# Performance work log

Measured on AMD Instinct MI355X. Metric: run time of the kernel, lower is better.

The kernel has to match this reference:

```python
import jax, jax.numpy as jnp
import numpy as np

DIM = 64
HEAD_DIM = 4
NUM_HEADS = DIM // HEAD_DIM  # 16
ATTN_DIM = NUM_HEADS * HEAD_DIM  # 64
BN_EPS = 1e-5


def setup_inputs() -> dict:
    key = jax.random.key(0)
    k_x, k_qkv, k_proj, k_g, k_b, k_m, k_v = jax.random.split(key, 7)
    B, C, H, W = 8, DIM, 64, 64
    x = jax.random.normal(k_x, (B, C, H, W), dtype=jnp.float32)
    # nn.Linear(dim, 3*attn_dim, bias=False): y = x @ W^T; store transposed for x @ w
    w_qkv = jax.random.normal(k_qkv, (DIM, 3 * ATTN_DIM), dtype=jnp.float32) * (DIM ** -0.5)
    w_proj = jax.random.normal(k_proj, (ATTN_DIM, DIM), dtype=jnp.float32) * (ATTN_DIM ** -0.5)
    gamma = 1.0 + 0.1 * jax.random.normal(k_g, (DIM,), dtype=jnp.float32)
    beta = 0.1 * jax.random.normal(k_b, (DIM,), dtype=jnp.float32)
    bn_mean = 0.1 * jax.random.normal(k_m, (DIM,), dtype=jnp.float32)
    bn_var = jnp.abs(jax.random.normal(k_v, (DIM,), dtype=jnp.float32)) + 0.5
    return {"x": x, "w_qkv": w_qkv, "w_proj": w_proj, "gamma": gamma,
            "beta": beta, "bn_mean": bn_mean, "bn_var": bn_var}


def _forward(x, w_qkv, w_proj, gamma, beta, bn_mean, bn_var):
    B, C, H, W = x.shape
    Hp, Wp = H // 2, W // 2
    N = Hp * Wp
    # ---- MaxPool2d(2,2) with indices (non-overlapping windows) ----
    xr = x.reshape(B, C, Hp, 2, Wp, 2).transpose(0, 1, 2, 4, 3, 5).reshape(B, C, Hp, Wp, 4)
    idx = jnp.argmax(xr, axis=-1)              # [B,C,Hp,Wp] window-local argmax
    pooled = jnp.max(xr, axis=-1)              # [B,C,Hp,Wp]
    # ---- GA attention on pooled map ----
    t = pooled.transpose(0, 2, 3, 1).reshape(B, N, C)          # [B,N,C]
    qkv = (t @ w_qkv).reshape(B, N, 3, NUM_HEADS, HEAD_DIM)
    q, k, v = qkv[:, :, 0], qkv[:, :, 1], qkv[:, :, 2]          # [B,N,h,d]
    scale = HEAD_DIM ** -0.5
    attn = jnp.einsum('bnhd,bmhd->bhnm', q, k) * scale          # [B,h,N,N]
    attn = jax.nn.softmax(attn, axis=-1)
    o = jnp.einsum('bhnm,bmhd->bnhd', attn, v).reshape(B, N, ATTN_DIM)
    o = (o @ w_proj).reshape(B, Hp, Wp, C).transpose(0, 3, 1, 2)  # [B,C,Hp,Wp]
    # ---- BatchNorm2d (eval mode, running stats) ----
    inv = gamma / jnp.sqrt(bn_var + BN_EPS)
    o = o * inv[:, None, None] + (beta - bn_mean * inv)[:, None, None]
    # ---- MaxUnpool2d(2,2): scatter to argmax positions ----
    oh = jax.nn.one_hot(idx, 4, dtype=o.dtype)                  # [B,C,Hp,Wp,4]
    up = oh * o[..., None]
    out = up.reshape(B, C, Hp, Wp, 2, 2).transpose(0, 1, 2, 4, 3, 5).reshape(B, C, H, W)
    return out


def reference(x, w_qkv, w_proj, gamma, beta, bn_mean, bn_var):
    return _forward(x, w_qkv, w_proj, gamma, beta, bn_mean, bn_var)
```

## Files before the change

kernel.cpp:

```cpp
#include <hip/hip_runtime.h>
#include <hip/hip_bf16.h>


typedef float    f32x4 __attribute__((ext_vector_type(4)));
typedef _Float16 f16x8 __attribute__((ext_vector_type(8)));
typedef unsigned int uint32_tt;

static __device__ __forceinline__ uint32_tt pk2(float a, float b) {
    uint32_tt lo = (uint32_tt)__builtin_bit_cast(unsigned short, (_Float16)a);
    uint32_tt hi = (uint32_tt)__builtin_bit_cast(unsigned short, (_Float16)b);
    return lo | (hi << 16);
}

__global__ __launch_bounds__(256) void pool_kernel(const float* __restrict__ x,
                                                   float* __restrict__ t,
                                                   int* __restrict__ idx) {
    int g = blockIdx.x * 256 + threadIdx.x;
    int wp = g & 31, hp = (g >> 5) & 31, c = (g >> 10) & 63, b = g >> 16;
    const float* px = x + (((b * 64 + c) * 64 + 2 * hp) * 64 + 2 * wp);
    float2 r0 = *(const float2*)px;
    float2 r1 = *(const float2*)(px + 64);
    float best = r0.x; int bi = 0;
    if (r0.y > best) { best = r0.y; bi = 1; }
    if (r1.x > best) { best = r1.x; bi = 2; }
    if (r1.y > best) { best = r1.y; bi = 3; }
    int n = hp * 32 + wp;
    t[(b * 64 + c) * 1024 + n] = best;
    idx[g] = bi;
}

__global__ __launch_bounds__(192) void qkv_kernel(const float* __restrict__ t,
                                                  const float* __restrict__ w_qkv,
                                                  float* __restrict__ q,
                                                  float* __restrict__ k,
                                                  float* __restrict__ v) {
    __shared__ float trow[16 * 68];
    int tid = threadIdx.x;
    int row0 = blockIdx.x * 16;
    {
        int b0 = row0 >> 10, n0 = row0 & 1023;
        for (int i = tid; i < 1024; i += 192) {
            int c = i >> 4, nn = i & 15;
            trow[nn * 68 + c] = t[(b0 * 64 + c) * 1024 + n0 + nn];
        }
    }
    int j  = tid % 96;
    int rh = tid / 96;
    float wc0[64], wc1[64];
    #pragma unroll
    for (int c = 0; c < 64; c++) {
        wc0[c] = w_qkv[c * 192 + j];
        wc1[c] = w_qkv[c * 192 + j + 96];
    }
    __syncthreads();
    int s0 = j >> 6, h0 = (j >> 2) & 15, d0 = j & 3;
    int j1 = j + 96;
    int s1 = j1 >> 6, h1 = (j1 >> 2) & 15, d1 = j1 & 3;
    float* dst0 = (s0 == 0) ? q : (s0 == 1) ? k : v;
    float* dst1 = (s1 == 0) ? q : (s1 == 1) ? k : v;
    for (int r = 0; r < 8; r++) {
        int row = rh * 8 + r;
        const float4* tr = (const float4*)&trow[row * 68];
        float a0 = 0.f, a1 = 0.f;
        #pragma unroll
        for (int c4 = 0; c4 < 16; c4++) {
            float4 tv = tr[c4];
            a0 += tv.x * wc0[c4 * 4] + tv.y * wc0[c4 * 4 + 1]
                + tv.z * wc0[c4 * 4 + 2] + tv.w * wc0[c4 * 4 + 3];
            a1 += tv.x * wc1[c4 * 4] + tv.y * wc1[c4 * 4 + 1]
                + tv.z * wc1[c4 * 4 + 2] + tv.w * wc1[c4 * 4 + 3];
        }
        int ng = row0 + row, b = ng >> 10, n = ng & 1023;
        dst0[((b * 16 + h0) * 1024 + n) * 4 + d0] = a0;
        dst1[((b * 16 + h1) * 1024 + n) * 4 + d1] = a1;
    }
}

__global__ __launch_bounds__(256) void prep_kernel(const float* __restrict__ k,
                                                   const float* __restrict__ v,
                                                   uint4* __restrict__ kg,
                                                   uint32_tt* __restrict__ vg) {
    int p = blockIdx.x;
    int bh = ((p & 7) << 4) | (p >> 3);
    int tid = threadIdx.x;
    const float4* kp4 = (const float4*)(k + bh * 4096);
    const float4* vp4 = (const float4*)(v + bh * 4096);
    uint4* kgb = kg + bh * 1024;
    uint32_tt* vgb = vg + bh * 2080;
    #pragma unroll
    for (int i = 0; i < 4; i++) {
        int key = i * 256 + tid;
        float4 kf = kp4[key];
        f16x8 kk;
        kk[0] = (_Float16)kf.x; kk[4] = (_Float16)(kf.x - (float)kk[0]);
        kk[1] = (_Float16)kf.y; kk[5] = (_Float16)(kf.y - (float)kk[1]);
        kk[2] = (_Float16)kf.z; kk[6] = (_Float16)(kf.z - (float)kk[2]);
        kk[3] = (_Float16)kf.w; kk[7] = (_Float16)(kf.w - (float)kk[3]);
        kgb[key] = __builtin_bit_cast(uint4, kk);
    }
    #pragma unroll
    for (int i = 0; i < 2; i++) {
        int m = i * 256 + tid;
        int key = 2 * m;
        float4 v0 = vp4[key], v1 = vp4[key + 1];
        int pos = (key & ~31) | (((key & 15) >> 2) << 3)
                | (((key >> 4) & 1) << 2) | (key & 3);
        int pw = pos >> 1;
        vgb[0 * 520 + pw] = pk2(v0.x, v1.x);
        vgb[1 * 520 + pw] = pk2(v0.y, v1.y);
        vgb[2 * 520 + pw] = pk2(v0.z, v1.z);
        vgb[3 * 520 + pw] = pk2(v0.w, v1.w);
    }
}

__global__ __launch_bounds__(256, 4) void attn_kernel(const float* __restrict__ q,
                                                      const uint4* __restrict__ kg,
                                                      const uint32_tt* __restrict__ vg,
                                                      float* __restrict__ o) {
    __shared__ __align__(16) unsigned char smem[27840];
    f16x8* Kh2 = (f16x8*)smem;
    float* lsc = (float*)(smem + 26752);
    int p = blockIdx.x;
    int xcd = p & 7, slot = p >> 3;
    int bh = (xcd << 4) | (slot >> 3);
    int row0 = (slot & 7) * 128;
    int tid = threadIdx.x;
    uint4* smem4 = (uint4*)smem;
    const uint4* kgb = kg + bh * 1024;
    const uint4* vgb = (const uint4*)(vg + bh * 2080);
    #pragma unroll
    for (int i = 0; i < 4; i++)
        smem4[i * 256 + tid] = kgb[i * 256 + tid];
    #pragma unroll
    for (int i = 0; i < 3; i++) {
        int ix = i * 256 + tid;
        if (ix < 520) smem4[1024 + ix] = vgb[ix];
    }
    {
        uint32_tt* op = (uint32_tt*)(smem + 24704);
        op[tid] = 0x3C003C00u;
        op[256 + tid] = 0x3C003C00u;
    }
    int w = tid >> 6, lane = tid & 63;
    int c = lane & 15, quad = lane >> 4;
    int mv = (c < 5) ? c : 4;
    const float C1 = 0.5f * 1.44269504088896f;
    const float4* qp4 = (const float4*)(q + bh * 4096);
    f16x8 bq[2];
    #pragma unroll
    for (int s = 0; s < 2; s++) {
        int rowg = row0 + w * 32 + s * 16 + c;
        float4 qv = qp4[rowg];
        float qx = qv.x * C1, qy = qv.y * C1, qz = qv.z * C1, qw = qv.w * C1;
        _Float16 hx = (_Float16)qx, hy = (_Float16)qy,
                 hz = (_Float16)qz, hw = (_Float16)qw;
        _Float16 gx = (_Float16)(qx - (float)hx), gy = (_Float16)(qy - (float)hy),
                 gz = (_Float16)(qz - (float)hz), gw = (_Float16)(qw - (float)hw);
        f16x8 a = {};
        if (quad == 0) {
            a[0] = hx; a[1] = hy; a[2] = hz; a[3] = hw;
            a[4] = hx; a[5] = hy; a[6] = hz; a[7] = hw;
        } else if (quad == 1) {
            a[0] = gx; a[1] = gy; a[2] = gz; a[3] = gw;
            a[4] = gx; a[5] = gy; a[6] = gz; a[7] = gw;
        }
        bq[s] = a;
    }
    __syncthreads();
    f32x4 acc[2];
    acc[0] = (f32x4)(0.f); acc[1] = (f32x4)(0.f);
    const f32x4 cm14 = { -14.f, -14.f, -14.f, -14.f };
    #pragma unroll 2
    for (int T = 0; T < 32; T++) {
        f16x8 ka0 = Kh2[(2 * T) * 16 + c];
        f16x8 ka1 = Kh2[(2 * T + 1) * 16 + c];
        const uint4* vptr = (const uint4*)(smem + 16384
                                           + mv * 2080 + T * 64 + quad * 16);
        f16x8 va = __builtin_bit_cast(f16x8, *vptr);
        #pragma unroll
        for (int s = 0; s < 2; s++) {
            f32x4 S0 = __builtin_amdgcn_mfma_f32_16x16x32_f16(ka0, bq[s], cm14, 0, 0, 0);
            f32x4 S1 = __builtin_amdgcn_mfma_f32_16x16x32_f16(ka1, bq[s], cm14, 0, 0, 0);
            float p00 = __builtin_amdgcn_exp2f(S0[0]);
            float p01 = __builtin_amdgcn_exp2f(S0[1]);
            float p02 = __builtin_amdgcn_exp2f(S0[2]);
            float p03 = __builtin_amdgcn_exp2f(S0[3]);
            float p10 = __builtin_amdgcn_exp2f(S1[0]);
            float p11 = __builtin_amdgcn_exp2f(S1[1]);
            float p12 = __builtin_amdgcn_exp2f(S1[2]);
            float p13 = __builtin_amdgcn_exp2f(S1[3]);
            uint4 pbu;
            pbu.x = __builtin_bit_cast(uint32_tt, __builtin_amdgcn_cvt_pkrtz(p00, p01));
            pbu.y = __builtin_bit_cast(uint32_tt, __builtin_amdgcn_cvt_pkrtz(p02, p03));
            pbu.z = __builtin_bit_cast(uint32_tt, __builtin_amdgcn_cvt_pkrtz(p10, p11));
            pbu.w = __builtin_bit_cast(uint32_tt, __builtin_amdgcn_cvt_pkrtz(p12, p13));
            f16x8 pb = __builtin_bit_cast(f16x8, pbu);
            acc[s] = __builtin_amdgcn_mfma_f32_16x16x32_f16(va, pb, acc[s], 0, 0, 0);
        }
    }
    if (quad == 1) {
        #pragma unroll
        for (int s = 0; s < 2; s++) lsc[w * 32 + s * 16 + c] = acc[s][0];
    }
    __syncthreads();
    if (quad == 0) {
        int b0 = bh >> 4, h = bh & 15;
        #pragma unroll
        for (int s = 0; s < 2; s++) {
            float rl = 1.f / lsc[w * 32 + s * 16 + c];
            int rowg = row0 + w * 32 + s * 16 + c;
            float4 res = { acc[s][0] * rl, acc[s][1] * rl,
                           acc[s][2] * rl, acc[s][3] * rl };
            *(float4*)&o[(b0 * 1024 + rowg) * 64 + h * 4] = res;
        }
    }
}

__global__ __launch_bounds__(256) void proj_kernel(const float* __restrict__ o,
                                                   const float* __restrict__ w_proj,
                                                   const float* __restrict__ gamma,
                                                   const float* __restrict__ beta,
                                                   const float* __restrict__ mean,
                                                   const float* __restrict__ var,
                                                   const int* __restrict__ idx,
                                                   float* __restrict__ out) {
    __shared__ float ws[64 * 64];
    int b = blockIdx.x >> 5, hp = blockIdx.x & 31;
    int tid = threadIdx.x;
    for (int i = tid; i < 4096; i += 256) ws[i] = w_proj[i];
    int wp = tid & 31, cg = tid >> 5;
    float oreg[64];
    const float* orow = o + (b * 1024 + hp * 32 + wp) * 64;
    #pragma unroll
    for (int a4 = 0; a4 < 16; a4++) {
        float4 t4 = ((const float4*)orow)[a4];
        oreg[a4 * 4] = t4.x; oreg[a4 * 4 + 1] = t4.y;
        oreg[a4 * 4 + 2] = t4.z; oreg[a4 * 4 + 3] = t4.w;
    }
    __syncthreads();
    #pragma unroll
    for (int g = 0; g < 2; g++) {
        int c0 = cg * 8 + g * 4;
        float4 acc = {0.f, 0.f, 0.f, 0.f};
        #pragma unroll
        for (int a = 0; a < 64; a++) {
            float4 wv = *(const float4*)&ws[a * 64 + c0];
            acc.x += oreg[a] * wv.x; acc.y += oreg[a] * wv.y;
            acc.z += oreg[a] * wv.z; acc.w += oreg[a] * wv.w;
        }
        float accs[4] = { acc.x, acc.y, acc.z, acc.w };
        #pragma unroll
        for (int i = 0; i < 4; i++) {
            int c = c0 + i;
            float inv = gamma[c] * rsqrtf(var[c] + 1e-5f);
            float val = accs[i] * inv + (beta[c] - mean[c] * inv);
            int id = idx[((b * 64 + c) * 32 + hp) * 32 + wp];
            int base = ((b * 64 + c) * 64 + 2 * hp) * 64 + 2 * wp;
            float2 r0 = { id == 0 ? val : 0.f, id == 1 ? val : 0.f };
            float2 r1 = { id == 2 ? val : 0.f, id == 3 ? val : 0.f };
            *(float2*)&out[base] = r0;
            *(float2*)&out[base + 64] = r1;
        }
    }
}

extern "C" void kernel_launch(void* const* d_in, const int* in_sizes, int n_in,
                              void* d_out, int out_size, void* d_ws, size_t ws_size,
                              hipStream_t stream) {
    const float* x      = (const float*)d_in[0];
    const float* w_qkv  = (const float*)d_in[1];
    const float* w_proj = (const float*)d_in[2];
    const float* gamma  = (const float*)d_in[3];
    const float* beta   = (const float*)d_in[4];
    const float* bn_mean= (const float*)d_in[5];
    const float* bn_var = (const float*)d_in[6];
    float* out = (float*)d_out;

    const int SEG = 524288;
    float* ws = (float*)d_ws;
    float* t   = ws;
    int*   idx = (int*)(ws + SEG);
    float* q   = ws + 2 * SEG;
    float* k   = ws + 3 * SEG;
    float* v   = ws + 4 * SEG;
    float* o   = ws + 5 * SEG;
    uint4*     kg = (uint4*)(ws + 6 * SEG);
    uint32_tt* vg = (uint32_tt*)(ws + 7 * SEG);

    pool_kernel<<<2048, 256, 0, stream>>>(x, t, idx);
    qkv_kernel<<<512, 192, 0, stream>>>(t, w_qkv, q, k, v);
    prep_kernel<<<128, 256, 0, stream>>>(k, v, kg, vg);
    attn_kernel<<<1024, 256, 0, stream>>>(q, kg, vg, o);
    proj_kernel<<<256, 256, 0, stream>>>(o, w_proj, gamma, beta, bn_mean, bn_var, idx, out);
}
```

Baseline: 114.9 us.

## Fuse maxpool, QKV projection and K/V fp16 packing into one kernel

Merges the pooling, QKV matmul and K/V prep kernels into one kernel that pools directly from x into shared memory, computes QKV, and writes packed K/V in the attention layout straight from LDS. This removes two launches and the global round-trips of the pooled map and the fp32 K/V buffers. Argmax indices shrink from int to bytes, and block ordering is interleaved over batch, including a proj_kernel index change. The trade-offs are more shared memory per block and scattered small stores for the idx and vg outputs.

```diff
diff --git a/kernel.cpp b/kernel.cpp
--- a/kernel.cpp
+++ b/kernel.cpp
@@ -12,38 +12,22 @@
     return lo | (hi << 16);
 }
 
-__global__ __launch_bounds__(256) void pool_kernel(const float* __restrict__ x,
-                                                   float* __restrict__ t,
-                                                   int* __restrict__ idx) {
-    int g = blockIdx.x * 256 + threadIdx.x;
-    int wp = g & 31, hp = (g >> 5) & 31, c = (g >> 10) & 63, b = g >> 16;
-    const float* px = x + (((b * 64 + c) * 64 + 2 * hp) * 64 + 2 * wp);
-    float2 r0 = *(const float2*)px;
-    float2 r1 = *(const float2*)(px + 64);
-    float best = r0.x; int bi = 0;
-    if (r0.y > best) { best = r0.y; bi = 1; }
-    if (r1.x > best) { best = r1.x; bi = 2; }
-    if (r1.y > best) { best = r1.y; bi = 3; }
-    int n = hp * 32 + wp;
-    t[(b * 64 + c) * 1024 + n] = best;
-    idx[g] = bi;
-}
-
-__global__ __launch_bounds__(192) void qkv_kernel(const float* __restrict__ t,
-                                                  const float* __restrict__ w_qkv,
-                                                  float* __restrict__ q,
-                                                  float* __restrict__ k,
-                                                  float* __restrict__ v) {
+__global__ __launch_bounds__(192) void fused_kernel(const float* __restrict__ x,
+                                                    const float* __restrict__ w_qkv,
+                                                    float* __restrict__ q,
+                                                    uint4* __restrict__ kg,
+                                                    uint32_tt* __restrict__ vg,
+                                                    unsigned char* __restrict__ idx) {
     __shared__ float trow[16 * 68];
+    __shared__ float kx[16 * 68];
+    __shared__ float vx[16 * 68];
     int tid = threadIdx.x;
-    int row0 = blockIdx.x * 16;
-    {
-        int b0 = row0 >> 10, n0 = row0 & 1023;
-        for (int i = tid; i < 1024; i += 192) {
-            int c = i >> 4, nn = i & 15;
-            trow[nn * 68 + c] = t[(b0 * 64 + c) * 1024 + n0 + nn];
-        }
-    }
+    int p = blockIdx.x;
+    int b = p & 7;
+    int tile = p >> 3;
+    int n0 = tile * 16;
+    int hp = n0 >> 5, wp0 = n0 & 31;
+
     int j  = tid % 96;
     int rh = tid / 96;
     float wc0[64], wc1[64];
@@ -52,12 +36,27 @@
         wc0[c] = w_qkv[c * 192 + j];
         wc1[c] = w_qkv[c * 192 + j + 96];
     }
-    __syncthreads();
+
+    for (int i = tid; i < 1024; i += 192) {
+        int c = i >> 4, nn = i & 15, wp = wp0 + nn;
+        const float* px = x + (((b * 64 + c) * 64 + 2 * hp) * 64 + 2 * wp);
+        float2 r0 = *(const float2*)px;
+        float2 r1 = *(const float2*)(px + 64);
+        float best = r0.x; int bi = 0;
+        if (r0.y > best) { best = r0.y; bi = 1; }
+        if (r1.x > best) { best = r1.x; bi = 2; }
+        if (r1.y > best) { best = r1.y; bi = 3; }
+        trow[nn * 68 + c] = best;
+        idx[((b * 64 + c) * 32 + hp) * 32 + wp] = (unsigned char)bi;
+    }
+    __syncthreads();
+
     int s0 = j >> 6, h0 = (j >> 2) & 15, d0 = j & 3;
     int j1 = j + 96;
-    int s1 = j1 >> 6, h1 = (j1 >> 2) & 15, d1 = j1 & 3;
-    float* dst0 = (s0 == 0) ? q : (s0 == 1) ? k : v;
-    float* dst1 = (s1 == 0) ? q : (s1 == 1) ? k : v;
+    int s1 = j1 >> 6;
+    int col0 = j & 63, col1 = j1 & 63;
+    float* xb0 = (s0 == 1) ? kx : vx;
+    float* xb1 = (s1 == 1) ? kx : vx;
     for (int r = 0; r < 8; r++) {
         int row = rh * 8 + r;
         const float4* tr = (const float4*)&trow[row * 68];
@@ -70,46 +69,31 @@
             a1 += tv.x * wc1[c4 * 4] + tv.y * wc1[c4 * 4 + 1]
                 + tv.z * wc1[c4 * 4 + 2] + tv.w * wc1[c4 * 4 + 3];
         }
-        int ng = row0 + row, b = ng >> 10, n = ng & 1023;
-        dst0[((b * 16 + h0) * 1024 + n) * 4 + d0] = a0;
-        dst1[((b * 16 + h1) * 1024 + n) * 4 + d1] = a1;
-    }
-}
-
-__global__ __launch_bounds__(256) void prep_kernel(const float* __restrict__ k,
-                                                   const float* __restrict__ v,
-                                                   uint4* __restrict__ kg,
-                                                   uint32_tt* __restrict__ vg) {
-    int p = blockIdx.x;
-    int bh = ((p & 7) << 4) | (p >> 3);
-    int tid = threadIdx.x;
-    const float4* kp4 = (const float4*)(k + bh * 4096);
-    const float4* vp4 = (const float4*)(v + bh * 4096);
-    uint4* kgb = kg + bh * 1024;
-    uint32_tt* vgb = vg + bh * 2080;
-    #pragma unroll
-    for (int i = 0; i < 4; i++) {
-        int key = i * 256 + tid;
-        float4 kf = kp4[key];
+        int n = n0 + row;
+        if (s0 == 0) q[((b * 16 + h0) * 1024 + n) * 4 + d0] = a0;
+        else         xb0[row * 68 + col0] = a0;
+        xb1[row * 68 + col1] = a1;
+    }
+    __syncthreads();
+
+    for (int e = tid; e < 256; e += 192) {
+        int kl = e & 15, h = e >> 4;
+        float4 kf = *(const float4*)&kx[kl * 68 + h * 4];
         f16x8 kk;
         kk[0] = (_Float16)kf.x; kk[4] = (_Float16)(kf.x - (float)kk[0]);
         kk[1] = (_Float16)kf.y; kk[5] = (_Float16)(kf.y - (float)kk[1]);
         kk[2] = (_Float16)kf.z; kk[6] = (_Float16)(kf.z - (float)kk[2]);
         kk[3] = (_Float16)kf.w; kk[7] = (_Float16)(kf.w - (float)kk[3]);
-        kgb[key] = __builtin_bit_cast(uint4, kk);
-    }
-    #pragma unroll
-    for (int i = 0; i < 2; i++) {
-        int m = i * 256 + tid;
-        int key = 2 * m;
-        float4 v0 = vp4[key], v1 = vp4[key + 1];
-        int pos = (key & ~31) | (((key & 15) >> 2) << 3)
-                | (((key >> 4) & 1) << 2) | (key & 3);
-        int pw = pos >> 1;
-        vgb[0 * 520 + pw] = pk2(v0.x, v1.x);
-        vgb[1 * 520 + pw] = pk2(v0.y, v1.y);
-        vgb[2 * 520 + pw] = pk2(v0.z, v1.z);
-        vgb[3 * 520 + pw] = pk2(v0.w, v1.w);
+        kg[(b * 16 + h) * 1024 + n0 + kl] = __builtin_bit_cast(uint4, kk);
+    }
+    int b4 = (n0 >> 4) & 1;
+    int pwbase = ((n0 & ~31) >> 1) + (b4 << 1);
+    for (int e = tid; e < 512; e += 192) {
+        int m = e & 7, h = (e >> 3) & 15, d = e >> 7;
+        float v0 = vx[(2 * m) * 68 + h * 4 + d];
+        float v1 = vx[(2 * m + 1) * 68 + h * 4 + d];
+        int pw = pwbase + ((m >> 1) << 2) + (m & 1);
+        vg[(b * 16 + h) * 2080 + d * 520 + pw] = pk2(v0, v1);
     }
 }
 
@@ -222,10 +206,11 @@
                                                    const float* __restrict__ beta,
                                                    const float* __restrict__ mean,
                                                    const float* __restrict__ var,
-                                                   const int* __restrict__ idx,
+                                                   const unsigned char* __restrict__ idx,
                                                    float* __restrict__ out) {
     __shared__ float ws[64 * 64];
-    int b = blockIdx.x >> 5, hp = blockIdx.x & 31;
+    int p = blockIdx.x;
+    int b = p & 7, hp = p >> 3;
     int tid = threadIdx.x;
     for (int i = tid; i < 4096; i += 256) ws[i] = w_proj[i];
     int wp = tid & 31, cg = tid >> 5;
@@ -278,18 +263,13 @@
 
     const int SEG = 524288;
     float* ws = (float*)d_ws;
-    float* t   = ws;
-    int*   idx = (int*)(ws + SEG);
+    unsigned char* idx = (unsigned char*)(ws + SEG);
     float* q   = ws + 2 * SEG;
-    float* k   = ws + 3 * SEG;
-    float* v   = ws + 4 * SEG;
     float* o   = ws + 5 * SEG;
     uint4*     kg = (uint4*)(ws + 6 * SEG);
     uint32_tt* vg = (uint32_tt*)(ws + 7 * SEG);
 
-    pool_kernel<<<2048, 256, 0, stream>>>(x, t, idx);
-    qkv_kernel<<<512, 192, 0, stream>>>(t, w_qkv, q, k, v);
-    prep_kernel<<<128, 256, 0, stream>>>(k, v, kg, vg);
+    fused_kernel<<<512, 192, 0, stream>>>(x, w_qkv, q, kg, vg, idx);
     attn_kernel<<<1024, 256, 0, stream>>>(q, kg, vg, o);
     proj_kernel<<<256, 256, 0, stream>>>(o, w_proj, gamma, beta, bn_mean, bn_var, idx, out);
 }
```

New measurement: 106.2 us. -7.6%, faster.
